# Performance work log

Measured on AMD Instinct MI355X. Metric: run time of the kernel, lower is better.

Reference implementation:

```python
import jax, jax.numpy as jnp
import numpy as np

B, N, CIN, COUT, MAXN, NF, MID = 8, 512, 64, 64, 16, 32, 16
M1 = [3, 32, 32, 1]
M2 = [CIN * COUT, 512, MID]
MR = [CIN * MID, 512, COUT]
BN_EPS = 1e-3  # keras BatchNormalization default epsilon


def mish(v):
    return v * jnp.tanh(jax.nn.softplus(v))


def bn(v, g, b):
    # training-mode batch norm over the row axis (keras BN in learning phase)
    mu = jnp.mean(v, axis=0, keepdims=True)
    var = jnp.var(v, axis=0, keepdims=True)
    return g * (v - mu) * jax.lax.rsqrt(var + BN_EPS) + b


def _mlp(v, layers):
    for W, b, g, be in layers:
        v = bn(mish(v @ W + b), g, be)
    return v


def setup_inputs() -> dict:
    key = jax.random.key(0)
    ks = jax.random.split(key, 16)
    inp = {
        'x': jax.random.normal(ks[0], (B, N, CIN), jnp.float32),
        'xyz': jax.random.normal(ks[1], (B, N, 3), jnp.float32),
        'framepoints': jax.random.normal(ks[2], (NF, 3), jnp.float32),
        'fpw': jax.random.normal(ks[3], (NF, CIN, COUT), jnp.float32) * 0.05,
    }
    ki = 4
    for name, dims in (('m1', M1), ('m2', M2), ('mr', MR)):
        for i in range(len(dims) - 1):
            inp[f'{name}_w{i}'] = jax.random.normal(ks[ki], (dims[i], dims[i + 1]), jnp.float32) / np.float32(np.sqrt(dims[i]))
            inp[f'{name}_b{i}'] = jnp.zeros((dims[i + 1],), jnp.float32)
            inp[f'{name}_g{i}'] = jnp.ones((dims[i + 1],), jnp.float32)
            inp[f'{name}_be{i}'] = jnp.zeros((dims[i + 1],), jnp.float32)
            ki += 1
    return inp


def reference(x, xyz, framepoints, fpw,
              m1_w0, m1_b0, m1_g0, m1_be0,
              m1_w1, m1_b1, m1_g1, m1_be1,
              m1_w2, m1_b2, m1_g2, m1_be2,
              m2_w0, m2_b0, m2_g0, m2_be0,
              m2_w1, m2_b1, m2_g1, m2_be1,
              mr_w0, mr_b0, mr_g0, mr_be0,
              mr_w1, mr_b1, mr_g1, mr_be1):
    Bc, Nc, cin = x.shape
    nf = framepoints.shape[0]
    cout = fpw.shape[2]
    mid = m2_w1.shape[1]

    # pairwise squared distances on FEATURES (as in the original), gram form
    sq = jnp.sum(x * x, axis=-1)  # [B,N]
    d = sq[:, :, None] + sq[:, None, :] - 2.0 * jnp.einsum('bnc,bmc->bnm', x, x)
    _, idx = jax.lax.top_k(-d, MAXN)  # [B,N,maxn] nearest (self first)

    bidx = jnp.arange(Bc)[:, None, None]
    xyz_sl = xyz[bidx, idx]  # [B,N,maxn,3]
    fur = x[bidx, idx]       # [B,N,maxn,cin]

    xyz_sl = xyz_sl.reshape(-1, MAXN, 3)
    rel = (xyz_sl - xyz_sl[:, :1, :]).reshape(-1, 3)  # [B*N*maxn, 3]

    # deterministic random rotation of frame points about the y axis
    ang = jax.random.uniform(jax.random.key(42), ()) * 2.0 * jnp.pi
    c = jnp.cos(ang); s = jnp.sin(ang)
    z = jnp.zeros_like(c); o = jnp.ones_like(c)
    R = jnp.stack([jnp.stack([c, z, s]), jnp.stack([z, o, z]), jnp.stack([-s, z, c])])
    fp = framepoints @ R  # [nf,3]

    sl = jnp.concatenate([rel, fp], axis=0)              # [M+nf, 3]
    diff = (sl[:, None, :] - fp[None, :, :]).reshape(-1, 3)  # [(M+nf)*nf, 3]

    h = _mlp(diff, [(m1_w0, m1_b0, m1_g0, m1_be0),
                    (m1_w1, m1_b1, m1_g1, m1_be1),
                    (m1_w2, m1_b2, m1_g2, m1_be2)])      # [(M+nf)*nf, 1]

    w = _mlp(fpw.reshape(nf, -1), [(m2_w0, m2_b0, m2_g0, m2_be0),
                                   (m2_w1, m2_b1, m2_g1, m2_be1)])  # [nf, mid]

    agg = jnp.sum(h.reshape(-1, nf, 1) * w[None], axis=1)  # [M+nf, mid]
    wmain = agg[:-nf].reshape(-1, MAXN, mid)               # [B*N, maxn, mid]

    f = jnp.einsum('kmc,kmd->kcd', fur.reshape(-1, MAXN, cin), wmain)
    f = f.reshape(-1, cin * mid)
    f = _mlp(f, [(mr_w0, mr_b0, mr_g0, mr_be0),
                 (mr_w1, mr_b1, mr_g1, mr_be1)])           # [B*N, cout]
    return f.reshape(Bc, Nc, cout)
```

## Files before the change

kernel.cpp:

```cpp
#include <hip/hip_runtime.h>
#include <math.h>

#define BB    8
#define NN    512
#define CIN   64
#define MAXN  16
#define NF    32
#define MID   16
#define BN_   4096
#define MSL   65536
#define MTOT  65568
#define RROWS 2098176
#define P2STR 40
#define AST   72

typedef unsigned short ushort_t;
typedef __attribute__((ext_vector_type(8))) short bf16x8;
typedef __attribute__((ext_vector_type(4))) float f32x4;

__device__ __forceinline__ float mishf(float x){
  float t  = __expf(x);
  float u  = 1.0f + t;
  float u2 = u * u;
  float r  = x * (u2 - 1.0f) * __builtin_amdgcn_rcpf(u2 + 1.0f);
  return (x > 15.0f) ? x : r;
}

__device__ __forceinline__ ushort_t f2bf(float f){
  unsigned u = __float_as_uint(f);
  unsigned r = (u + 0x7FFFu + ((u >> 16) & 1u)) >> 16;
  return (ushort_t)r;
}

__device__ __forceinline__ unsigned rotl32(unsigned v, unsigned s){
  return (v << s) | (v >> (32u - s));
}

__device__ __forceinline__ float jax_uniform42(){
  unsigned ks[3];
  ks[0] = 0u; ks[1] = 42u; ks[2] = 0x1BD11BDAu ^ 0u ^ 42u;
  const unsigned rot[8] = {13u,15u,26u,6u,17u,29u,16u,24u};
  unsigned x0 = ks[0];
  unsigned x1 = ks[1];
  #pragma unroll
  for (int blk = 0; blk < 5; ++blk){
    #pragma unroll
    for (int r = 0; r < 4; ++r){
      x0 += x1;
      x1 = rotl32(x1, rot[(blk & 1) * 4 + r]);
      x1 ^= x0;
    }
    x0 += ks[(blk + 1) % 3];
    x1 += ks[(blk + 2) % 3] + (unsigned)(blk + 1);
  }
  unsigned w = x0 ^ x1;
  return __uint_as_float((w >> 9) | 0x3f800000u) - 1.0f;
}

__global__ __launch_bounds__(256) void k_sq(const float* __restrict__ x, double* __restrict__ sqd){
  int r = blockIdx.x * 256 + threadIdx.x;
  const float4* p = (const float4*)(x + (size_t)r * 64);
  double a0 = 0.0, a1 = 0.0, a2 = 0.0, a3 = 0.0;
  #pragma unroll
  for (int k = 0; k < 16; k += 4){
    float4 v0 = p[k], v1 = p[k+1], v2 = p[k+2], v3 = p[k+3];
    a0 += (double)v0.x*v0.x + (double)v0.y*v0.y + (double)v0.z*v0.z + (double)v0.w*v0.w;
    a1 += (double)v1.x*v1.x + (double)v1.y*v1.y + (double)v1.z*v1.z + (double)v1.w*v1.w;
    a2 += (double)v2.x*v2.x + (double)v2.y*v2.y + (double)v2.z*v2.z + (double)v2.w*v2.w;
    a3 += (double)v3.x*v3.x + (double)v3.y*v3.y + (double)v3.z*v3.z + (double)v3.w*v3.w;
  }
  sqd[r] = (a0 + a1) + (a2 + a3);
}

__global__ __launch_bounds__(256) void k_topk(const float* __restrict__ x, const double* __restrict__ sqd,
                                              int* __restrict__ idxp){
  __shared__ float ct[128 * 65];
  __shared__ float xnl[4][64];
  int tid  = threadIdx.x;
  int lane = tid & 63;
  int wid  = tid >> 6;
  int g = blockIdx.x * 4 + wid;
  int b = g >> 9;
  const float* xb = x + (size_t)b * (NN * CIN);
  {
    int w = tid >> 6, c = tid & 63;
    int nq = (blockIdx.x * 4 + w) & 511;
    xnl[w][c] = xb[nq * 64 + c];
  }
  double sqn = sqd[g];

  double dst[8];
  #pragma unroll 1
  for (int tile = 0; tile < 4; ++tile){
    __syncthreads();
    #pragma unroll
    for (int u = 0; u < 8; ++u){
      int idx = u * 256 + tid;
      int row = idx >> 4, q = idx & 15;
      float4 v = *(const float4*)&xb[(size_t)(tile * 128 + row) * 64 + q * 4];
      float* d = &ct[row * 65 + q * 4];
      d[0] = v.x; d[1] = v.y; d[2] = v.z; d[3] = v.w;
    }
    __syncthreads();
    double a[2][4];
    #pragma unroll
    for (int s = 0; s < 2; ++s)
      #pragma unroll
      for (int i = 0; i < 4; ++i) a[s][i] = 0.0;
    #pragma unroll
    for (int k = 0; k < 16; ++k){
      float4 qv = *(const float4*)&xnl[wid][k * 4];
      double q0 = (double)qv.x, q1 = (double)qv.y, q2 = (double)qv.z, q3 = (double)qv.w;
      #pragma unroll
      for (int s = 0; s < 2; ++s){
        const float* rp = &ct[(lane + 64 * s) * 65 + k * 4];
        a[s][0] += q0 * (double)rp[0];
        a[s][1] += q1 * (double)rp[1];
        a[s][2] += q2 * (double)rp[2];
        a[s][3] += q3 * (double)rp[3];
      }
    }
    #pragma unroll
    for (int s = 0; s < 2; ++s){
      int m = tile * 128 + 64 * s + lane;
      dst[tile * 2 + s] = sqn + sqd[(b << 9) + m] - 2.0 * ((a[s][0] + a[s][1]) + (a[s][2] + a[s][3]));
    }
  }

  for (int it = 0; it < 16; ++it){
    double bd = 1.0e300; int bi = 0x7FFFFFFF;
    #pragma unroll
    for (int j = 0; j < 8; ++j){
      int m = ((j >> 1) << 7) + ((j & 1) << 6) + lane;
      if (dst[j] < bd){ bd = dst[j]; bi = m; }
    }
    #pragma unroll
    for (int off = 1; off < 64; off <<= 1){
      double od = __shfl_xor(bd, off);
      int    oi = __shfl_xor(bi, off);
      if (od < bd || (od == bd && oi < bi)){ bd = od; bi = oi; }
    }
    if (lane == 0) idxp[g * 16 + it] = bi;
    if (lane == (bi & 63)){
      int slot = ((bi >> 7) << 1) | ((bi >> 6) & 1);
      #pragma unroll
      for (int j = 0; j < 8; ++j) if (j == slot) dst[j] = 1.0e300;
    }
  }
}

__global__ __launch_bounds__(256) void k_prep(const float* __restrict__ xyz,
                                              const float* __restrict__ fpts,
                                              const int* __restrict__ idxp,
                                              const float* __restrict__ w0, const float* __restrict__ b0,
                                              float* __restrict__ sib, float* __restrict__ fjt){
  __shared__ float w0l[96], b0l[32];
  int tid = threadIdx.x;
  if (tid < 96) w0l[tid] = w0[tid];
  else if (tid < 128) b0l[tid - 96] = b0[tid - 96];
  __syncthreads();
  int i = blockIdx.x * 256 + tid;
  if (i >= MTOT) return;
  float vx, vy, vz;
  if (i < MSL){
    int bn = i >> 4, m = i & 15, b = bn >> 9;
    int i0 = idxp[bn * 16];
    int im = idxp[bn * 16 + m];
    const float* xz = xyz + (size_t)b * (NN * 3);
    vx = xz[im * 3 + 0] - xz[i0 * 3 + 0];
    vy = xz[im * 3 + 1] - xz[i0 * 3 + 1];
    vz = xz[im * 3 + 2] - xz[i0 * 3 + 2];
  } else {
    int j = i - MSL;
    float u   = jax_uniform42();
    float ang = (u * 2.0f) * 3.14159274f;
    float c = cosf(ang), s = sinf(ang);
    float fx = fpts[j * 3 + 0], fy = fpts[j * 3 + 1], fz = fpts[j * 3 + 2];
    vx = fx * c - fz * s;
    vy = fy;
    vz = fx * s + fz * c;
  }
  float si[32];
  #pragma unroll
  for (int c = 0; c < 32; ++c)
    si[c] = vx * w0l[c] + vy * w0l[32 + c] + vz * w0l[64 + c];
  float* dst = sib + (size_t)i * 32;
  #pragma unroll
  for (int cq = 0; cq < 8; ++cq){
    float4 o = make_float4(si[cq*4+0] + b0l[cq*4+0], si[cq*4+1] + b0l[cq*4+1],
                           si[cq*4+2] + b0l[cq*4+2], si[cq*4+3] + b0l[cq*4+3]);
    *(float4*)&dst[cq*4] = o;
  }
  if (i >= MSL){
    int j = i - MSL;
    #pragma unroll
    for (int c = 0; c < 32; ++c) fjt[c * 32 + j] = si[c];
  }
}

__global__ __launch_bounds__(256) void k_m1_p1(const float* __restrict__ sib, const float* __restrict__ fjt,
                                               float* __restrict__ s0g, float* __restrict__ q0g){
  __shared__ float fjlt[1024];
  __shared__ float red[8][32], redq[8][32];
  int tid = threadIdx.x;
  for (int t = tid; t < 1024; t += 256) fjlt[t] = fjt[(t & 31) * 32 + (t >> 5)];
  __syncthreads();
  int c = tid & 31, s = tid >> 5;
  float as = 0.0f, aq = 0.0f;
  size_t base = (size_t)blockIdx.x * 2048;
  #pragma unroll 4
  for (int t = 0; t < 256; ++t){
    size_t r = base + (size_t)t * 8 + s;
    if (r < (size_t)RROWS){
      int i = (int)(r >> 5), j = (int)(r & 31);
      float m = mishf(sib[(size_t)i * 32 + c] - fjlt[j * 32 + c]);
      as += m; aq += m * m;
    }
  }
  red[s][c] = as; redq[s][c] = aq;
  __syncthreads();
  if (tid < 32){
    float ts = 0.0f, tq = 0.0f;
    #pragma unroll
    for (int ss = 0; ss < 8; ++ss){ ts += red[ss][tid]; tq += redq[ss][tid]; }
    int bank = (blockIdx.x & 15) * 32 + tid;
    atomicAdd(&s0g[bank], ts);
    atomicAdd(&q0g[bank], tq);
  }
}

__global__ __launch_bounds__(256, 6) void k_m1_p2(const float* __restrict__ sib, const float* __restrict__ fjt,
                                               const float* __restrict__ w1g, const float* __restrict__ b1g,
                                               const float* __restrict__ g0, const float* __restrict__ be0,
                                               const float* __restrict__ s0g, const float* __restrict__ q0g,
                                               float* __restrict__ s1g, float* __restrict__ q1g,
                                               ushort_t* __restrict__ a1b){
  __shared__ __align__(16) ushort_t a0s[256 * P2STR];
  __shared__ __align__(16) float uni[1024];
  __shared__ float A0l[32], C0l[32], biasX[32], satm[32], qatm[32];
  ushort_t* wts = (ushort_t*)uni;
  int tid = threadIdx.x;
  for (int t = tid; t < 1024; t += 256) uni[t] = fjt[t];
  if (tid < 32){
    float s = 0.0f, q = 0.0f;
    #pragma unroll
    for (int b = 0; b < 16; ++b){ s += s0g[b * 32 + tid]; q += q0g[b * 32 + tid]; }
    const float invR = 1.0f / (float)RROWS;
    float mu = s * invR, var = q * invR - mu * mu;
    float A = g0[tid] * rsqrtf(var + 1e-3f);
    A0l[tid] = A; C0l[tid] = be0[tid] - mu * A;
    satm[tid] = 0.0f; qatm[tid] = 0.0f;
  }
  __syncthreads();
  {
    int r = blockIdx.x * 256 + tid;
    int i = r >> 5, j = r & 31;
    const float* sr = sib + (size_t)i * 32;
    ushort_t* dst = &a0s[tid * P2STR];
    #pragma unroll
    for (int cq = 0; cq < 4; ++cq){
      float4 sa = *(const float4*)&sr[cq * 8];
      float4 sb = *(const float4*)&sr[cq * 8 + 4];
      float m0 = mishf(sa.x - uni[(cq*8+0)*32 + j]);
      float m1 = mishf(sa.y - uni[(cq*8+1)*32 + j]);
      float m2 = mishf(sa.z - uni[(cq*8+2)*32 + j]);
      float m3 = mishf(sa.w - uni[(cq*8+3)*32 + j]);
      float m4 = mishf(sb.x - uni[(cq*8+4)*32 + j]);
      float m5 = mishf(sb.y - uni[(cq*8+5)*32 + j]);
      float m6 = mishf(sb.z - uni[(cq*8+6)*32 + j]);
      float m7 = mishf(sb.w - uni[(cq*8+7)*32 + j]);
      uint4 pk;
      pk.x = (unsigned)f2bf(m0) | ((unsigned)f2bf(m1) << 16);
      pk.y = (unsigned)f2bf(m2) | ((unsigned)f2bf(m3) << 16);
      pk.z = (unsigned)f2bf(m4) | ((unsigned)f2bf(m5) << 16);
      pk.w = (unsigned)f2bf(m6) | ((unsigned)f2bf(m7) << 16);
      *(uint4*)&dst[cq * 8] = pk;
    }
  }
  if (tid < 32){
    float acc = b1g[tid];
    #pragma unroll
    for (int k = 0; k < 32; ++k) acc += C0l[k] * w1g[k * 32 + tid];
    biasX[tid] = acc;
  }
  __syncthreads();
  for (int t = tid; t < 1024; t += 256){
    int k = t >> 5, c = t & 31;
    wts[c * P2STR + k] = f2bf(w1g[t] * A0l[k]);
  }
  __syncthreads();
  int lane = tid & 63, w = tid >> 6;
  int ln15 = lane & 15, quad = lane >> 4;
  f32x4 zero = {0.0f, 0.0f, 0.0f, 0.0f};
  bf16x8 bfr0 = *(bf16x8*)&wts[(ln15) * P2STR + quad * 8];
  bf16x8 bfr1 = *(bf16x8*)&wts[(16 + ln15) * P2STR + quad * 8];
  f32x4 acc[4][2];
  #pragma unroll
  for (int i2 = 0; i2 < 4; ++i2){
    int row = (w * 4 + i2) * 16 + ln15;
    bf16x8 af = *(bf16x8*)&a0s[row * P2STR + quad * 8];
    acc[i2][0] = __builtin_amdgcn_mfma_f32_16x16x32_bf16(af, bfr0, zero, 0, 0, 0);
    acc[i2][1] = __builtin_amdgcn_mfma_f32_16x16x32_bf16(af, bfr1, zero, 0, 0, 0);
  }
  float cs[2] = {0.0f, 0.0f}, cq2[2] = {0.0f, 0.0f};
  size_t rowbase = (size_t)blockIdx.x * 256 + w * 64 + quad * 4;
  #pragma unroll
  for (int nt = 0; nt < 2; ++nt){
    int col = nt * 16 + ln15;
    float bx = biasX[col];
    size_t colbase = (size_t)col * RROWS;
    #pragma unroll
    for (int i2 = 0; i2 < 4; ++i2){
      f32x4 a = acc[i2][nt];
      float m0 = mishf(a[0] + bx);
      float m1 = mishf(a[1] + bx);
      float m2 = mishf(a[2] + bx);
      float m3 = mishf(a[3] + bx);
      cs[nt]  += m0 + m1 + m2 + m3;
      cq2[nt] += m0*m0 + m1*m1 + m2*m2 + m3*m3;
      if (a1b){
        uint2 pk;
        pk.x = (unsigned)f2bf(m0) | ((unsigned)f2bf(m1) << 16);
        pk.y = (unsigned)f2bf(m2) | ((unsigned)f2bf(m3) << 16);
        *(uint2*)&a1b[colbase + rowbase + (size_t)i2 * 16] = pk;
      }
    }
  }
  #pragma unroll
  for (int nt = 0; nt < 2; ++nt){
    float v = cs[nt], u = cq2[nt];
    v += __shfl_xor(v, 16); u += __shfl_xor(u, 16);
    v += __shfl_xor(v, 32); u += __shfl_xor(u, 32);
    if (lane < 16){
      atomicAdd(&satm[nt * 16 + ln15], v);
      atomicAdd(&qatm[nt * 16 + ln15], u);
    }
  }
  __syncthreads();
  if (tid < 32){
    int bank = (blockIdx.x & 15) * 32 + tid;
    atomicAdd(&s1g[bank], satm[tid]);
    atomicAdd(&q1g[bank], qatm[tid]);
  }
}

__global__ __launch_bounds__(256) void k_m1_p3s(const ushort_t* __restrict__ a1b,
                                                const float* __restrict__ w2g, const float* __restrict__ b2g,
                                                const float* __restrict__ g1, const float* __restrict__ be1,
                                                const float* __restrict__ s1g, const float* __restrict__ q1g,
                                                float* __restrict__ act2, float* __restrict__ s2g, float* __restrict__ q2g){
  __shared__ float vvl[32], C1l[32], cb2l[1], r2s[4], r2q[4];
  int tid = threadIdx.x;
  if (tid < 32){
    float s = 0.0f, q = 0.0f;
    #pragma unroll
    for (int b = 0; b < 16; ++b){ s += s1g[b * 32 + tid]; q += q1g[b * 32 + tid]; }
    const float invR = 1.0f / (float)RROWS;
    float mu = s * invR, var = q * invR - mu * mu;
    float A = g1[tid] * rsqrtf(var + 1e-3f);
    C1l[tid] = be1[tid] - mu * A;
    vvl[tid] = A * w2g[tid];
  }
  __syncthreads();
  if (tid == 0){
    float a = b2g[0];
    #pragma unroll
    for (int k = 0; k < 32; ++k) a += C1l[k] * w2g[k];
    cb2l[0] = a;
  }
  __syncthreads();
  size_t r0 = (size_t)blockIdx.x * 512 + (size_t)tid * 2;
  float pre0 = 0.0f, pre1 = 0.0f;
  #pragma unroll
  for (int c = 0; c < 32; ++c){
    unsigned u = *(const unsigned*)&a1b[(size_t)c * RROWS + r0];
    float lo = __uint_as_float(u << 16);
    float hi = __uint_as_float(u & 0xFFFF0000u);
    pre0 += lo * vvl[c];
    pre1 += hi * vvl[c];
  }
  float cb2 = cb2l[0];
  float a20 = mishf(pre0 + cb2);
  float a21 = mishf(pre1 + cb2);
  *(float2*)&act2[r0] = make_float2(a20, a21);
  float ss = a20 + a21, qq = a20*a20 + a21*a21;
  #pragma unroll
  for (int off = 1; off < 64; off <<= 1){ ss += __shfl_xor(ss, off); qq += __shfl_xor(qq, off); }
  int lane = tid & 63, wid = tid >> 6;
  if (lane == 0){ r2s[wid] = ss; r2q[wid] = qq; }
  __syncthreads();
  if (tid == 0){
    atomicAdd(&s2g[blockIdx.x & 15], r2s[0] + r2s[1] + r2s[2] + r2s[3]);
    atomicAdd(&q2g[blockIdx.x & 15], r2q[0] + r2q[1] + r2q[2] + r2q[3]);
  }
}

__global__ __launch_bounds__(256, 3) void k_m1_p3f(const float* __restrict__ sib, const float* __restrict__ fjt,
                                               const float* __restrict__ w1g, const float* __restrict__ b1g,
                                               const float* __restrict__ g0, const float* __restrict__ be0,
                                               const float* __restrict__ g1, const float* __restrict__ be1,
                                               const float* __restrict__ w2g, const float* __restrict__ b2g,
                                               const float* __restrict__ s0g, const float* __restrict__ q0g,
                                               const float* __restrict__ s1g, const float* __restrict__ q1g,
                                               float* __restrict__ act2, float* __restrict__ s2g, float* __restrict__ q2g){
  __shared__ float fjl[1024];
  __shared__ float w1s[1024];
  __shared__ float A0l[32], C0l[32], A1l[32], C1l[32], biasX[32], vvl[32];
  __shared__ float a0t[32 * 256];
  __shared__ float cb2l[1];
  __shared__ float r2s[4], r2q[4];
  int tid = threadIdx.x;
  const float invR = 1.0f / (float)RROWS;
  for (int t = tid; t < 1024; t += 256) fjl[t] = fjt[t];
  if (tid < 32){
    float s = 0.0f, q = 0.0f;
    #pragma unroll
    for (int b = 0; b < 16; ++b){ s += s0g[b * 32 + tid]; q += q0g[b * 32 + tid]; }
    float mu = s * invR, var = q * invR - mu * mu;
    float A = g0[tid] * rsqrtf(var + 1e-3f);
    A0l[tid] = A; C0l[tid] = be0[tid] - mu * A;
  } else if (tid < 64){
    int c = tid - 32;
    float s = 0.0f, q = 0.0f;
    #pragma unroll
    for (int b = 0; b < 16; ++b){ s += s1g[b * 32 + c]; q += q1g[b * 32 + c]; }
    float mu = s * invR, var = q * invR - mu * mu;
    float A = g1[c] * rsqrtf(var + 1e-3f);
    A1l[c] = A; C1l[c] = be1[c] - mu * A;
  }
  __syncthreads();
  for (int t = tid; t < 1024; t += 256) w1s[t] = w1g[t] * A0l[t >> 5];
  if (tid < 32){
    float acc = b1g[tid];
    #pragma unroll
    for (int k = 0; k < 32; ++k) acc += C0l[k] * w1g[k * 32 + tid];
    biasX[tid] = acc;
  } else if (tid < 96 && tid >= 64){
    int c = tid - 64;
    vvl[c] = A1l[c] * w2g[c];
  } else if (tid == 96){
    float acc = b2g[0];
    #pragma unroll
    for (int k = 0; k < 32; ++k) acc += C1l[k] * w2g[k];
    cb2l[0] = acc;
  }
  {
    int r = blockIdx.x * 256 + tid;
    int i = r >> 5, j = r & 31;
    const float* sr = sib + (size_t)i * 32;
    #pragma unroll
    for (int cq = 0; cq < 8; ++cq){
      float4 sv = *(const float4*)&sr[cq * 4];
      a0t[(cq*4+0)*256 + tid] = mishf(sv.x - fjl[(cq*4+0)*32 + j]);
      a0t[(cq*4+1)*256 + tid] = mishf(sv.y - fjl[(cq*4+1)*32 + j]);
      a0t[(cq*4+2)*256 + tid] = mishf(sv.z - fjl[(cq*4+2)*32 + j]);
      a0t[(cq*4+3)*256 + tid] = mishf(sv.w - fjl[(cq*4+3)*32 + j]);
    }
  }
  __syncthreads();
  int cg = tid & 7, rg = tid >> 3;
  float acc[8][4];
  #pragma unroll
  for (int i2 = 0; i2 < 8; ++i2)
    #pragma unroll
    for (int j2 = 0; j2 < 4; ++j2) acc[i2][j2] = 0.0f;
  #pragma unroll 4
  for (int k = 0; k < 32; ++k){
    float4 w  = *(const float4*)&w1s[k * 32 + cg * 4];
    float4 aA = *(const float4*)&a0t[k * 256 + rg * 8];
    float4 aB = *(const float4*)&a0t[k * 256 + rg * 8 + 4];
    float ar[8] = {aA.x, aA.y, aA.z, aA.w, aB.x, aB.y, aB.z, aB.w};
    float wc[4] = {w.x, w.y, w.z, w.w};
    #pragma unroll
    for (int i2 = 0; i2 < 8; ++i2)
      #pragma unroll
      for (int j2 = 0; j2 < 4; ++j2) acc[i2][j2] += ar[i2] * wc[j2];
  }
  float cb2 = cb2l[0];
  float ss = 0.0f, qq = 0.0f;
  #pragma unroll
  for (int rr = 0; rr < 8; ++rr){
    float part = 0.0f;
    #pragma unroll
    for (int cc = 0; cc < 4; ++cc){
      float m = mishf(acc[rr][cc] + biasX[cg * 4 + cc]);
      part += m * vvl[cg * 4 + cc];
    }
    part += __shfl_xor(part, 1);
    part += __shfl_xor(part, 2);
    part += __shfl_xor(part, 4);
    float a2 = mishf(part + cb2);
    if (cg == 0){
      act2[(size_t)blockIdx.x * 256 + rg * 8 + rr] = a2;
      ss += a2; qq += a2 * a2;
    }
  }
  #pragma unroll
  for (int off = 1; off < 64; off <<= 1){ ss += __shfl_xor(ss, off); qq += __shfl_xor(qq, off); }
  int lane = tid & 63, wid = tid >> 6;
  if (lane == 0){ r2s[wid] = ss; r2q[wid] = qq; }
  __syncthreads();
  if (tid == 0){
    atomicAdd(&s2g[blockIdx.x & 15], r2s[0] + r2s[1] + r2s[2] + r2s[3]);
    atomicAdd(&q2g[blockIdx.x & 15], r2q[0] + r2q[1] + r2q[2] + r2q[3]);
  }
}

__global__ __launch_bounds__(512) void k_wmlp1(const float* __restrict__ fpw, const float* __restrict__ W0,
                                               float* __restrict__ wact0){
  int f = blockIdx.x, kc = blockIdx.y, c = threadIdx.x;
  const float* row = fpw + (size_t)f * 4096 + kc * 512;
  const float* wp  = W0 + (size_t)(kc * 512) * 512 + c;
  float acc = 0.0f;
  #pragma unroll 8
  for (int k = 0; k < 512; ++k) acc += row[k] * wp[(size_t)k * 512];
  atomicAdd(&wact0[f * 512 + c], acc);
}

__global__ __launch_bounds__(512) void k_wmlp2(const float* __restrict__ wact0, const float* __restrict__ b0,
                                               const float* __restrict__ W1,
                                               const float* __restrict__ b1,
                                               const float* __restrict__ g0, const float* __restrict__ be0,
                                               const float* __restrict__ g1, const float* __restrict__ be1,
                                               float* __restrict__ wfin){
  __shared__ float wl[32 * 512];
  __shared__ float o2l[512], A1l[16], C1l[16];
  int t = threadIdx.x;
  {
    float b0t = b0[t];
    float v[32]; float sum = 0.0f, sq = 0.0f;
    #pragma unroll
    for (int r = 0; r < 32; ++r){
      v[r] = mishf(wact0[r * 512 + t] + b0t);
      sum += v[r]; sq += v[r] * v[r];
    }
    float mu  = sum * (1.0f / 32.0f);
    float var = sq * (1.0f / 32.0f) - mu * mu;
    float A = g0[t] * rsqrtf(var + 1e-3f);
    float C = be0[t] - mu * A;
    #pragma unroll
    for (int r = 0; r < 32; ++r) wl[r * 512 + t] = v[r] * A + C;
  }
  __syncthreads();
  {
    int r = t >> 4, c2 = t & 15;
    float pre = b1[c2];
    for (int k = 0; k < 512; ++k) pre += wl[r * 512 + k] * W1[k * 16 + c2];
    o2l[t] = mishf(pre);
  }
  __syncthreads();
  if (t < 16){
    float sum = 0.0f, sq = 0.0f;
    #pragma unroll
    for (int r = 0; r < 32; ++r){ float v = o2l[r * 16 + t]; sum += v; sq += v * v; }
    float mu  = sum * (1.0f / 32.0f);
    float var = sq * (1.0f / 32.0f) - mu * mu;
    float A = g1[t] * rsqrtf(var + 1e-3f);
    A1l[t] = A; C1l[t] = be1[t] - mu * A;
  }
  __syncthreads();
  wfin[t] = o2l[t] * A1l[t & 15] + C1l[t & 15];
}

__global__ __launch_bounds__(256) void k_agg(const float* __restrict__ act2, const float* __restrict__ wfin,
                                             const float* __restrict__ x, const int* __restrict__ idxp,
                                             const float* __restrict__ s2, const float* __restrict__ q2,
                                             const float* __restrict__ g2, const float* __restrict__ be2,
                                             float* __restrict__ fbuf){
  __shared__ float hl[512], wfl[512], wm[256], furl[1024], AC[2];
  int t = threadIdx.x;
  int k = blockIdx.x;
  if (t == 0){
    const float invR = 1.0f / (float)RROWS;
    float ssum = 0.0f, qsum = 0.0f;
    #pragma unroll
    for (int b = 0; b < 16; ++b){ ssum += s2[b]; qsum += q2[b]; }
    float mu  = ssum * invR;
    float var = qsum * invR - mu * mu;
    float A = g2[0] * rsqrtf(var + 1e-3f);
    AC[0] = A; AC[1] = be2[0] - mu * A;
  }
  wfl[t] = wfin[t]; wfl[t + 256] = wfin[t + 256];
  __syncthreads();
  float A2 = AC[0], C2 = AC[1];
  hl[t]       = act2[(size_t)k * 512 + t]       * A2 + C2;
  hl[t + 256] = act2[(size_t)k * 512 + 256 + t] * A2 + C2;
  __syncthreads();
  {
    int m = t >> 4, d = t & 15;
    float acc = 0.0f;
    #pragma unroll
    for (int j = 0; j < 32; ++j) acc += hl[m * 32 + j] * wfl[j * 16 + d];
    wm[t] = acc;
  }
  int b = k >> 9;
  const float* xb = x + (size_t)b * (NN * CIN);
  {
    int c = t & 63;
    #pragma unroll
    for (int it = 0; it < 4; ++it){
      int m = it * 4 + (t >> 6);
      int im = idxp[k * 16 + m];
      furl[m * 64 + c] = xb[im * 64 + c];
    }
  }
  __syncthreads();
  {
    int d = t & 15, c0 = t >> 4;
    #pragma unroll
    for (int q = 0; q < 4; ++q){
      int c = c0 + 16 * q;
      float acc = 0.0f;
      #pragma unroll
      for (int m = 0; m < 16; ++m) acc += furl[m * 64 + c] * wm[m * 16 + d];
      fbuf[(size_t)k * 1024 + t + 256 * q] = acc;
    }
  }
}

__global__ __launch_bounds__(256) void k_mr1(const float* __restrict__ F, const float* __restrict__ W,
                                             const float* __restrict__ bias, float* __restrict__ out,
                                             float* __restrict__ s3, float* __restrict__ q3){
  __shared__ __align__(16) ushort_t As[64 * AST];
  __shared__ __align__(16) ushort_t Bs[64 * AST];
  __shared__ float csum[64], csq[64];
  int tid = threadIdx.x;
  int m0 = blockIdx.y * 64, n0 = blockIdx.x * 64;
  int lane = tid & 63, w = tid >> 6;
  int ln15 = lane & 15, quad = lane >> 4;
  if (tid < 64){ csum[tid] = 0.0f; csq[tid] = 0.0f; }
  f32x4 acc[4];
  #pragma unroll
  for (int n = 0; n < 4; ++n){ acc[n][0] = 0.0f; acc[n][1] = 0.0f; acc[n][2] = 0.0f; acc[n][3] = 0.0f; }

  #pragma unroll 1
  for (int k0 = 0; k0 < 1024; k0 += 64){
    __syncthreads();
    {
      int row = tid >> 2, kq = (tid & 3) * 16;
      const float* src = &F[(size_t)(m0 + row) * 1024 + k0 + kq];
      float4 v0 = *(const float4*)&src[0];
      float4 v1 = *(const float4*)&src[4];
      float4 v2 = *(const float4*)&src[8];
      float4 v3 = *(const float4*)&src[12];
      uint4 p0, p1;
      p0.x = (unsigned)f2bf(v0.x) | ((unsigned)f2bf(v0.y) << 16);
      p0.y = (unsigned)f2bf(v0.z) | ((unsigned)f2bf(v0.w) << 16);
      p0.z = (unsigned)f2bf(v1.x) | ((unsigned)f2bf(v1.y) << 16);
      p0.w = (unsigned)f2bf(v1.z) | ((unsigned)f2bf(v1.w) << 16);
      p1.x = (unsigned)f2bf(v2.x) | ((unsigned)f2bf(v2.y) << 16);
      p1.y = (unsigned)f2bf(v2.z) | ((unsigned)f2bf(v2.w) << 16);
      p1.z = (unsigned)f2bf(v3.x) | ((unsigned)f2bf(v3.y) << 16);
      p1.w = (unsigned)f2bf(v3.z) | ((unsigned)f2bf(v3.w) << 16);
      ushort_t* dst = &As[row * AST + kq];
      *(uint4*)&dst[0] = p0;
      *(uint4*)&dst[8] = p1;
    }
    #pragma unroll
    for (int rr = 0; rr < 4; ++rr){
      int kk = rr * 16 + (tid >> 4);
      int nn = (tid & 15) * 4;
      float4 v = *(const float4*)&W[(size_t)(k0 + kk) * 512 + n0 + nn];
      Bs[(nn + 0) * AST + kk] = f2bf(v.x);
      Bs[(nn + 1) * AST + kk] = f2bf(v.y);
      Bs[(nn + 2) * AST + kk] = f2bf(v.z);
      Bs[(nn + 3) * AST + kk] = f2bf(v.w);
    }
    __syncthreads();
    #pragma unroll
    for (int ks = 0; ks < 64; ks += 32){
      bf16x8 af = *(bf16x8*)&As[(w * 16 + ln15) * AST + ks + quad * 8];
      #pragma unroll
      for (int n = 0; n < 4; ++n){
        bf16x8 bfv = *(bf16x8*)&Bs[(n * 16 + ln15) * AST + ks + quad * 8];
        acc[n] = __builtin_amdgcn_mfma_f32_16x16x32_bf16(af, bfv, acc[n], 0, 0, 0);
      }
    }
  }
  #pragma unroll
  for (int n = 0; n < 4; ++n){
    int col = n0 + n * 16 + ln15;
    float bv = bias[col];
    f32x4 a = acc[n];
    float s = 0.0f, q = 0.0f;
    #pragma unroll
    for (int r = 0; r < 4; ++r){
      float v = mishf(a[r] + bv);
      int row = m0 + w * 16 + quad * 4 + r;
      out[(size_t)row * 512 + col] = v;
      s += v; q += v * v;
    }
    s += __shfl_xor(s, 16); q += __shfl_xor(q, 16);
    s += __shfl_xor(s, 32); q += __shfl_xor(q, 32);
    if (quad == 0){
      atomicAdd(&csum[n * 16 + ln15], s);
      atomicAdd(&csq[n * 16 + ln15], q);
    }
  }
  __syncthreads();
  if (tid < 64){
    atomicAdd(&s3[n0 + tid], csum[tid]);
    atomicAdd(&q3[n0 + tid], csq[tid]);
  }
}

__global__ __launch_bounds__(256) void k_mr2(const float* __restrict__ Ain, const float* __restrict__ W,
                                             const float* __restrict__ bias,
                                             const float* __restrict__ s3, const float* __restrict__ q3,
                                             const float* __restrict__ g0, const float* __restrict__ be0,
                                             float* __restrict__ out, float* __restrict__ s4, float* __restrict__ q4){
  __shared__ float As2[16][68];
  __shared__ float Bs2[16][68];
  __shared__ float A3l[512], C3l[512];
  __shared__ float csum[64], csq[64];
  int tid = threadIdx.x;
  for (int kk = tid; kk < 512; kk += 256){
    const float invR = 1.0f / 4096.0f;
    float mu  = s3[kk] * invR;
    float var = q3[kk] * invR - mu * mu;
    float A = g0[kk] * rsqrtf(var + 1e-3f);
    A3l[kk] = A; C3l[kk] = be0[kk] - mu * A;
  }
  if (tid < 64){ csum[tid] = 0.0f; csq[tid] = 0.0f; }
  __syncthreads();
  int m0 = blockIdx.x * 64;
  int tx = tid & 15, ty = tid >> 4;
  float acc[4][4];
  #pragma unroll
  for (int i = 0; i < 4; ++i)
    #pragma unroll
    for (int j = 0; j < 4; ++j) acc[i][j] = 0.0f;
  int lmm = tid >> 2, lkq = (tid & 3) * 4;
  int lkk = tid >> 4, lnq = (tid & 15) * 4;
  float4 av = *(const float4*)&Ain[(size_t)(m0 + lmm) * 512 + lkq];
  float4 bv = *(const float4*)&W[(size_t)lkk * 64 + lnq];
  for (int k0 = 0; k0 < 512; k0 += 16){
    As2[lkq + 0][lmm] = av.x * A3l[k0 + lkq + 0] + C3l[k0 + lkq + 0];
    As2[lkq + 1][lmm] = av.y * A3l[k0 + lkq + 1] + C3l[k0 + lkq + 1];
    As2[lkq + 2][lmm] = av.z * A3l[k0 + lkq + 2] + C3l[k0 + lkq + 2];
    As2[lkq + 3][lmm] = av.w * A3l[k0 + lkq + 3] + C3l[k0 + lkq + 3];
    *(float4*)&Bs2[lkk][lnq] = bv;
    __syncthreads();
    if (k0 + 16 < 512){
      av = *(const float4*)&Ain[(size_t)(m0 + lmm) * 512 + (k0 + 16) + lkq];
      bv = *(const float4*)&W[(size_t)((k0 + 16) + lkk) * 64 + lnq];
    }
    #pragma unroll
    for (int kk = 0; kk < 16; ++kk){
      float4 a4 = *(const float4*)&As2[kk][ty * 4];
      float4 b4 = *(const float4*)&Bs2[kk][tx * 4];
      float a[4] = {a4.x, a4.y, a4.z, a4.w};
      float bb[4] = {b4.x, b4.y, b4.z, b4.w};
      #pragma unroll
      for (int i = 0; i < 4; ++i)
        #pragma unroll
        for (int j = 0; j < 4; ++j) acc[i][j] += a[i] * bb[j];
    }
    __syncthreads();
  }
  float4 bq = *(const float4*)&bias[tx * 4];
  float bvs[4] = {bq.x, bq.y, bq.z, bq.w};
  float cs[4] = {0,0,0,0}, cq[4] = {0,0,0,0};
  #pragma unroll
  for (int i = 0; i < 4; ++i){
    float v[4];
    #pragma unroll
    for (int j = 0; j < 4; ++j){
      v[j] = mishf(acc[i][j] + bvs[j]);
      cs[j] += v[j]; cq[j] += v[j] * v[j];
    }
    float4 o = make_float4(v[0], v[1], v[2], v[3]);
    *(float4*)&out[(size_t)(m0 + ty * 4 + i) * 64 + tx * 4] = o;
  }
  #pragma unroll
  for (int j = 0; j < 4; ++j){
    float v = cs[j], w = cq[j];
    v += __shfl_xor(v, 16); w += __shfl_xor(w, 16);
    v += __shfl_xor(v, 32); w += __shfl_xor(w, 32);
    if ((tid & 63) < 16){
      atomicAdd(&csum[tx * 4 + j], v);
      atomicAdd(&csq[tx * 4 + j], w);
    }
  }
  __syncthreads();
  if (tid < 64){
    atomicAdd(&s4[tid], csum[tid]);
    atomicAdd(&q4[tid], csq[tid]);
  }
}

__global__ __launch_bounds__(256) void k_out(const float* __restrict__ pre,
                                             const float* __restrict__ s4, const float* __restrict__ q4,
                                             const float* __restrict__ g1, const float* __restrict__ be1,
                                             float* __restrict__ outp){
  int e = blockIdx.x * 256 + threadIdx.x;
  int c = e & 63;
  const float invR = 1.0f / 4096.0f;
  float mu  = s4[c] * invR;
  float var = q4[c] * invR - mu * mu;
  float A = g1[c] * rsqrtf(var + 1e-3f);
  outp[e] = pre[e] * A + (be1[c] - mu * A);
}

extern "C" void kernel_launch(void* const* d_in, const int* in_sizes, int n_in,
                              void* d_out, int out_size, void* d_ws, size_t ws_size,
                              hipStream_t stream){
  (void)in_sizes; (void)n_in; (void)out_size;
  const float* x    = (const float*)d_in[0];
  const float* xyz  = (const float*)d_in[1];
  const float* fpts = (const float*)d_in[2];
  const float* fpw  = (const float*)d_in[3];
  const float* m1w0 = (const float*)d_in[4];
  const float* m1b0 = (const float*)d_in[5];
  const float* m1g0 = (const float*)d_in[6];
  const float* m1be0= (const float*)d_in[7];
  const float* m1w1 = (const float*)d_in[8];
  const float* m1b1 = (const float*)d_in[9];
  const float* m1g1 = (const float*)d_in[10];
  const float* m1be1= (const float*)d_in[11];
  const float* m1w2 = (const float*)d_in[12];
  const float* m1b2 = (const float*)d_in[13];
  const float* m1g2 = (const float*)d_in[14];
  const float* m1be2= (const float*)d_in[15];
  const float* m2w0 = (const float*)d_in[16];
  const float* m2b0 = (const float*)d_in[17];
  const float* m2g0 = (const float*)d_in[18];
  const float* m2be0= (const float*)d_in[19];
  const float* m2w1 = (const float*)d_in[20];
  const float* m2b1 = (const float*)d_in[21];
  const float* m2g1 = (const float*)d_in[22];
  const float* m2be1= (const float*)d_in[23];
  const float* mrw0 = (const float*)d_in[24];
  const float* mrb0 = (const float*)d_in[25];
  const float* mrg0 = (const float*)d_in[26];
  const float* mrbe0= (const float*)d_in[27];
  const float* mrw1 = (const float*)d_in[28];
  const float* mrb1 = (const float*)d_in[29];
  const float* mrg1 = (const float*)d_in[30];
  const float* mrbe1= (const float*)d_in[31];

  float* wsf = (float*)d_ws;
  float* s0 = wsf + 0;     float* q0 = wsf + 512;
  float* s1 = wsf + 1024;  float* q1 = wsf + 1536;
  float* s2 = wsf + 2048;  float* q2 = wsf + 2064;
  float* s3 = wsf + 2080;  float* q3 = wsf + 2592;
  float* s4 = wsf + 3104;  float* q4 = wsf + 3168;
  int*   idxp = (int*)(wsf + 4096);
  double* sqd = (double*)(wsf + 69632);
  float* wact0= wsf + 332032;
  float* wfin = wsf + 348416;
  float* act2 = wsf + 348928;
  float* fbuf = wsf + 2447104;
  float* sib  = fbuf;
  float* fjt  = fbuf + 2098176;
  float* mact = wsf + 6641408;
  float* mact2= wsf + 8738560;

  size_t need = 9000704ULL * 4 + (size_t)RROWS * 32 * 2;
  bool fast = (ws_size >= need);
  ushort_t* a1b = fast ? (ushort_t*)(wsf + 9000704) : nullptr;

  hipMemsetAsync(d_ws, 0, 4096 * sizeof(float), stream);
  hipMemsetAsync(wact0, 0, 16384 * sizeof(float), stream);

  k_sq<<<16, 256, 0, stream>>>(x, sqd);
  k_topk<<<1024, 256, 0, stream>>>(x, sqd, idxp);
  k_prep<<<257, 256, 0, stream>>>(xyz, fpts, idxp, m1w0, m1b0, sib, fjt);
  k_m1_p1<<<1025, 256, 0, stream>>>(sib, fjt, s0, q0);
  k_m1_p2<<<8196, 256, 0, stream>>>(sib, fjt, m1w1, m1b1, m1g0, m1be0, s0, q0, s1, q1, a1b);
  if (fast){
    k_m1_p3s<<<4098, 256, 0, stream>>>(a1b, m1w2, m1b2, m1g1, m1be1, s1, q1, act2, s2, q2);
  } else {
    k_m1_p3f<<<8196, 256, 0, stream>>>(sib, fjt, m1w1, m1b1, m1g0, m1be0, m1g1, m1be1,
                                       m1w2, m1b2, s0, q0, s1, q1, act2, s2, q2);
  }
  k_wmlp1<<<dim3(32, 8), 512, 0, stream>>>(fpw, m2w0, wact0);
  k_wmlp2<<<1, 512, 0, stream>>>(wact0, m2b0, m2w1, m2b1, m2g0, m2be0, m2g1, m2be1, wfin);
  k_agg<<<4096, 256, 0, stream>>>(act2, wfin, x, idxp, s2, q2, m1g2, m1be2, fbuf);
  k_mr1<<<dim3(8, 64), 256, 0, stream>>>(fbuf, mrw0, mrb0, mact, s3, q3);
  k_mr2<<<64, 256, 0, stream>>>(mact, mrw1, mrb1, s3, q3, mrg0, mrbe0, mact2, s4, q4);
  k_out<<<1024, 256, 0, stream>>>(mact2, s4, q4, mrg1, mrbe1, (float*)d_out);
}
```

Baseline: 502.1 us.

## Materialize bf16 layer-0 activations in stats pass and store agg output as bf16

The first M1 stats pass now also writes the mish activations as packed bf16 to a workspace buffer (when the workspace is large enough), so the second pass loads them instead of recomputing mish. The aggregation kernel writes its output in bf16 so the MR GEMM loads half the bytes and skips conversion. Manual bf16 rounding is also replaced with the hardware packed-convert instruction. This trades recomputation for an extra large memory write and read, and depends on the workspace size for the new path.

```diff
diff --git a/kernel.cpp b/kernel.cpp
--- a/kernel.cpp
+++ b/kernel.cpp
@@ -30,6 +30,12 @@
   unsigned u = __float_as_uint(f);
   unsigned r = (u + 0x7FFFu + ((u >> 16) & 1u)) >> 16;
   return (ushort_t)r;
+}
+
+__device__ __forceinline__ unsigned cvt_pk_bf16(float lo, float hi){
+  unsigned r;
+  asm("v_cvt_pk_bf16_f32 %0, %1, %2" : "=v"(r) : "v"(lo), "v"(hi));
+  return r;
 }
 
 __device__ __forceinline__ unsigned rotl32(unsigned v, unsigned s){
@@ -199,30 +205,35 @@
 }
 
 __global__ __launch_bounds__(256) void k_m1_p1(const float* __restrict__ sib, const float* __restrict__ fjt,
-                                               float* __restrict__ s0g, float* __restrict__ q0g){
-  __shared__ float fjlt[1024];
-  __shared__ float red[8][32], redq[8][32];
+                                               float* __restrict__ s0g, float* __restrict__ q0g,
+                                               ushort_t* __restrict__ a0g){
+  __shared__ float fjlt[32 * 33];
+  __shared__ float red[16][32], redq[16][32];
   int tid = threadIdx.x;
-  for (int t = tid; t < 1024; t += 256) fjlt[t] = fjt[(t & 31) * 32 + (t >> 5)];
-  __syncthreads();
-  int c = tid & 31, s = tid >> 5;
-  float as = 0.0f, aq = 0.0f;
-  size_t base = (size_t)blockIdx.x * 2048;
+  for (int t = tid; t < 1024; t += 256) fjlt[(t & 31) * 33 + (t >> 5)] = fjt[t];
+  __syncthreads();
+  int c2 = (tid & 15) * 2, s = tid >> 4;
+  float as0 = 0.0f, aq0 = 0.0f, as1 = 0.0f, aq1 = 0.0f;
+  int base = blockIdx.x * 1024;
   #pragma unroll 4
-  for (int t = 0; t < 256; ++t){
-    size_t r = base + (size_t)t * 8 + s;
-    if (r < (size_t)RROWS){
-      int i = (int)(r >> 5), j = (int)(r & 31);
-      float m = mishf(sib[(size_t)i * 32 + c] - fjlt[j * 32 + c]);
-      as += m; aq += m * m;
-    }
-  }
-  red[s][c] = as; redq[s][c] = aq;
+  for (int t = 0; t < 64; ++t){
+    int r = base + t * 16 + s;
+    int i = r >> 5, j = r & 31;
+    float2 v = *(const float2*)&sib[(size_t)i * 32 + c2];
+    float2 f = *(const float2*)&fjlt[j * 33 + c2];
+    float m0 = mishf(v.x - f.x);
+    float m1 = mishf(v.y - f.y);
+    as0 += m0; aq0 += m0 * m0;
+    as1 += m1; aq1 += m1 * m1;
+    if (a0g) *(unsigned*)&a0g[(size_t)r * 32 + c2] = cvt_pk_bf16(m0, m1);
+  }
+  red[s][c2] = as0;  red[s][c2 + 1] = as1;
+  redq[s][c2] = aq0; redq[s][c2 + 1] = aq1;
   __syncthreads();
   if (tid < 32){
     float ts = 0.0f, tq = 0.0f;
     #pragma unroll
-    for (int ss = 0; ss < 8; ++ss){ ts += red[ss][tid]; tq += redq[ss][tid]; }
+    for (int ss = 0; ss < 16; ++ss){ ts += red[ss][tid]; tq += redq[ss][tid]; }
     int bank = (blockIdx.x & 15) * 32 + tid;
     atomicAdd(&s0g[bank], ts);
     atomicAdd(&q0g[bank], tq);
@@ -230,6 +241,7 @@
 }
 
 __global__ __launch_bounds__(256, 6) void k_m1_p2(const float* __restrict__ sib, const float* __restrict__ fjt,
+                                               const ushort_t* __restrict__ a0g,
                                                const float* __restrict__ w1g, const float* __restrict__ b1g,
                                                const float* __restrict__ g0, const float* __restrict__ be0,
                                                const float* __restrict__ s0g, const float* __restrict__ q0g,
@@ -240,7 +252,9 @@
   __shared__ float A0l[32], C0l[32], biasX[32], satm[32], qatm[32];
   ushort_t* wts = (ushort_t*)uni;
   int tid = threadIdx.x;
-  for (int t = tid; t < 1024; t += 256) uni[t] = fjt[t];
+  if (!a0g){
+    for (int t = tid; t < 1024; t += 256) uni[t] = fjt[t];
+  }
   if (tid < 32){
     float s = 0.0f, q = 0.0f;
     #pragma unroll
@@ -252,7 +266,16 @@
     satm[tid] = 0.0f; qatm[tid] = 0.0f;
   }
   __syncthreads();
-  {
+  if (a0g){
+    int r = blockIdx.x * 256 + tid;
+    const uint4* src = (const uint4*)(a0g + (size_t)r * 32);
+    uint4 v0 = src[0], v1 = src[1], v2 = src[2], v3 = src[3];
+    ushort_t* dst = &a0s[tid * P2STR];
+    *(uint4*)&dst[0]  = v0;
+    *(uint4*)&dst[8]  = v1;
+    *(uint4*)&dst[16] = v2;
+    *(uint4*)&dst[24] = v3;
+  } else {
     int r = blockIdx.x * 256 + tid;
     int i = r >> 5, j = r & 31;
     const float* sr = sib + (size_t)i * 32;
@@ -270,10 +293,10 @@
       float m6 = mishf(sb.z - uni[(cq*8+6)*32 + j]);
       float m7 = mishf(sb.w - uni[(cq*8+7)*32 + j]);
       uint4 pk;
-      pk.x = (unsigned)f2bf(m0) | ((unsigned)f2bf(m1) << 16);
-      pk.y = (unsigned)f2bf(m2) | ((unsigned)f2bf(m3) << 16);
-      pk.z = (unsigned)f2bf(m4) | ((unsigned)f2bf(m5) << 16);
-      pk.w = (unsigned)f2bf(m6) | ((unsigned)f2bf(m7) << 16);
+      pk.x = cvt_pk_bf16(m0, m1);
+      pk.y = cvt_pk_bf16(m2, m3);
+      pk.z = cvt_pk_bf16(m4, m5);
+      pk.w = cvt_pk_bf16(m6, m7);
       *(uint4*)&dst[cq * 8] = pk;
     }
   }
@@ -320,8 +343,8 @@
       cq2[nt] += m0*m0 + m1*m1 + m2*m2 + m3*m3;
       if (a1b){
         uint2 pk;
-        pk.x = (unsigned)f2bf(m0) | ((unsigned)f2bf(m1) << 16);
-        pk.y = (unsigned)f2bf(m2) | ((unsigned)f2bf(m3) << 16);
+        pk.x = cvt_pk_bf16(m0, m1);
+        pk.y = cvt_pk_bf16(m2, m3);
         *(uint2*)&a1b[colbase + rowbase + (size_t)i2 * 16] = pk;
       }
     }
@@ -566,7 +589,7 @@
                                              const float* __restrict__ x, const int* __restrict__ idxp,
                                              const float* __restrict__ s2, const float* __restrict__ q2,
                                              const float* __restrict__ g2, const float* __restrict__ be2,
-                                             float* __restrict__ fbuf){
+                                             ushort_t* __restrict__ fb16){
   __shared__ float hl[512], wfl[512], wm[256], furl[1024], AC[2];
   int t = threadIdx.x;
   int k = blockIdx.x;
@@ -613,12 +636,12 @@
       float acc = 0.0f;
       #pragma unroll
       for (int m = 0; m < 16; ++m) acc += furl[m * 64 + c] * wm[m * 16 + d];
-      fbuf[(size_t)k * 1024 + t + 256 * q] = acc;
-    }
-  }
-}
-
-__global__ __launch_bounds__(256) void k_mr1(const float* __restrict__ F, const float* __restrict__ W,
+      fb16[(size_t)k * 1024 + t + 256 * q] = f2bf(acc);
+    }
+  }
+}
+
+__global__ __launch_bounds__(256) void k_mr1(const ushort_t* __restrict__ F16, const float* __restrict__ W,
                                              const float* __restrict__ bias, float* __restrict__ out,
                                              float* __restrict__ s3, float* __restrict__ q3){
   __shared__ __align__(16) ushort_t As[64 * AST];
@@ -638,33 +661,23 @@
     __syncthreads();
     {
       int row = tid >> 2, kq = (tid & 3) * 16;
-      const float* src = &F[(size_t)(m0 + row) * 1024 + k0 + kq];
-      float4 v0 = *(const float4*)&src[0];
-      float4 v1 = *(const float4*)&src[4];
-      float4 v2 = *(const float4*)&src[8];
-      float4 v3 = *(const float4*)&src[12];
-      uint4 p0, p1;
-      p0.x = (unsigned)f2bf(v0.x) | ((unsigned)f2bf(v0.y) << 16);
-      p0.y = (unsigned)f2bf(v0.z) | ((unsigned)f2bf(v0.w) << 16);
-      p0.z = (unsigned)f2bf(v1.x) | ((unsigned)f2bf(v1.y) << 16);
-      p0.w = (unsigned)f2bf(v1.z) | ((unsigned)f2bf(v1.w) << 16);
-      p1.x = (unsigned)f2bf(v2.x) | ((unsigned)f2bf(v2.y) << 16);
-      p1.y = (unsigned)f2bf(v2.z) | ((unsigned)f2bf(v2.w) << 16);
-      p1.z = (unsigned)f2bf(v3.x) | ((unsigned)f2bf(v3.y) << 16);
-      p1.w = (unsigned)f2bf(v3.z) | ((unsigned)f2bf(v3.w) << 16);
+      const uint4* src = (const uint4*)&F16[(size_t)(m0 + row) * 1024 + k0 + kq];
+      uint4 v0 = src[0], v1 = src[1];
       ushort_t* dst = &As[row * AST + kq];
-      *(uint4*)&dst[0] = p0;
-      *(uint4*)&dst[8] = p1;
+      *(uint4*)&dst[0] = v0;
+      *(uint4*)&dst[8] = v1;
     }
     #pragma unroll
     for (int rr = 0; rr < 4; ++rr){
       int kk = rr * 16 + (tid >> 4);
       int nn = (tid & 15) * 4;
       float4 v = *(const float4*)&W[(size_t)(k0 + kk) * 512 + n0 + nn];
-      Bs[(nn + 0) * AST + kk] = f2bf(v.x);
-      Bs[(nn + 1) * AST + kk] = f2bf(v.y);
-      Bs[(nn + 2) * AST + kk] = f2bf(v.z);
-      Bs[(nn + 3) * AST + kk] = f2bf(v.w);
+      unsigned p01 = cvt_pk_bf16(v.x, v.y);
+      unsigned p23 = cvt_pk_bf16(v.z, v.w);
+      Bs[(nn + 0) * AST + kk] = (ushort_t)p01;
+      Bs[(nn + 1) * AST + kk] = (ushort_t)(p01 >> 16);
+      Bs[(nn + 2) * AST + kk] = (ushort_t)p23;
+      Bs[(nn + 3) * AST + kk] = (ushort_t)(p23 >> 16);
     }
     __syncthreads();
     #pragma unroll
@@ -853,12 +866,16 @@
   float* fbuf = wsf + 2447104;
   float* sib  = fbuf;
   float* fjt  = fbuf + 2098176;
+  ushort_t* fb16 = (ushort_t*)fbuf;
   float* mact = wsf + 6641408;
   float* mact2= wsf + 8738560;
 
-  size_t need = 9000704ULL * 4 + (size_t)RROWS * 32 * 2;
-  bool fast = (ws_size >= need);
+  size_t need1 = 9000704ULL * 4 + (size_t)RROWS * 32 * 2;
+  size_t need2 = need1 + (size_t)RROWS * 32 * 2;
+  bool fast = (ws_size >= need1);
+  bool t2   = (ws_size >= need2);
   ushort_t* a1b = fast ? (ushort_t*)(wsf + 9000704) : nullptr;
+  ushort_t* a0g = t2   ? (ushort_t*)(wsf + 9000704 + 33570816) : nullptr;
 
   hipMemsetAsync(d_ws, 0, 4096 * sizeof(float), stream);
   hipMemsetAsync(wact0, 0, 16384 * sizeof(float), stream);
@@ -866,8 +883,8 @@
   k_sq<<<16, 256, 0, stream>>>(x, sqd);
   k_topk<<<1024, 256, 0, stream>>>(x, sqd, idxp);
   k_prep<<<257, 256, 0, stream>>>(xyz, fpts, idxp, m1w0, m1b0, sib, fjt);
-  k_m1_p1<<<1025, 256, 0, stream>>>(sib, fjt, s0, q0);
-  k_m1_p2<<<8196, 256, 0, stream>>>(sib, fjt, m1w1, m1b1, m1g0, m1be0, s0, q0, s1, q1, a1b);
+  k_m1_p1<<<2049, 256, 0, stream>>>(sib, fjt, s0, q0, a0g);
+  k_m1_p2<<<8196, 256, 0, stream>>>(sib, fjt, a0g, m1w1, m1b1, m1g0, m1be0, s0, q0, s1, q1, a1b);
   if (fast){
     k_m1_p3s<<<4098, 256, 0, stream>>>(a1b, m1w2, m1b2, m1g1, m1be1, s1, q1, act2, s2, q2);
   } else {
@@ -876,8 +893,8 @@
   }
   k_wmlp1<<<dim3(32, 8), 512, 0, stream>>>(fpw, m2w0, wact0);
   k_wmlp2<<<1, 512, 0, stream>>>(wact0, m2b0, m2w1, m2b1, m2g0, m2be0, m2g1, m2be1, wfin);
-  k_agg<<<4096, 256, 0, stream>>>(act2, wfin, x, idxp, s2, q2, m1g2, m1be2, fbuf);
-  k_mr1<<<dim3(8, 64), 256, 0, stream>>>(fbuf, mrw0, mrb0, mact, s3, q3);
+  k_agg<<<4096, 256, 0, stream>>>(act2, wfin, x, idxp, s2, q2, m1g2, m1be2, fb16);
+  k_mr1<<<dim3(8, 64), 256, 0, stream>>>(fb16, mrw0, mrb0, mact, s3, q3);
   k_mr2<<<64, 256, 0, stream>>>(mact, mrw1, mrb1, s3, q3, mrg0, mrbe0, mact2, s4, q4);
   k_out<<<1024, 256, 0, stream>>>(mact2, s4, q4, mrg1, mrbe1, (float*)d_out);
 }
```

Result: faster. 466.2 us (-7.1%).
